# Kernel tuning notes

Measured on AMD Instinct MI355X. Metric: run time of the kernel, lower is better.

## Reference

```python
import jax, jax.numpy as jnp
import numpy as np

W_DIM = 512
IN_CH = 512
OUT_CH = 512
K = 3
PAD = K // 2
LR_MUL = 1.0
WEIGHT_GAIN = LR_MUL / np.sqrt(IN_CH * K * K)
MOD_WEIGHT_GAIN = 1.0 / np.sqrt(W_DIM)  # EqualizedLinear lr_mul=1.0
MOD_BIAS_GAIN = 1.0


def setup_inputs() -> dict:
    key = jax.random.key(0)
    k1, k2, k3, k4 = jax.random.split(key, 4)
    x = jax.random.normal(k1, (16, IN_CH, 64, 64), dtype=jnp.float32)
    w = jax.random.normal(k2, (16, W_DIM), dtype=jnp.float32)
    weight = jax.random.normal(k3, (OUT_CH, IN_CH, K, K), dtype=jnp.float32) / LR_MUL
    mod_weight = jax.random.normal(k4, (IN_CH, W_DIM), dtype=jnp.float32)
    mod_bias = jnp.ones((IN_CH,), dtype=jnp.float32)  # bias_init=1.0
    return {"x": x, "w": w, "weight": weight, "mod_weight": mod_weight, "mod_bias": mod_bias}


def _conv_one(xi, wi):
    # xi: [C_in, H, W], wi: [C_out, C_in, K, K]
    out = jax.lax.conv_general_dilated(
        xi[None], wi, window_strides=(1, 1),
        padding=[(PAD, PAD), (PAD, PAD)],
        dimension_numbers=("NCHW", "OIHW", "NCHW"))
    return out[0]


def reference(x, w, weight, mod_weight, mod_bias):
    # style = EqualizedLinear(w): [B, C_in]
    style = w @ (mod_weight * MOD_WEIGHT_GAIN).T + mod_bias * MOD_BIAS_GAIN
    # modulate weights per-sample: [B, C_out, C_in, K, K]
    wmod = (weight * WEIGHT_GAIN)[None] * style[:, None, :, None, None]
    # demodulate
    demod = jax.lax.rsqrt(jnp.sum(jnp.square(wmod), axis=(2, 3, 4), keepdims=True) + 1e-8)
    wmod = wmod * demod
    # per-sample conv (groups=batch in the original) via vmap
    out = jax.vmap(_conv_one)(x, wmod)  # [B, C_out, H, W]
    return out
```

## Files before the change

### kernel.cpp

```cpp
#include <hip/hip_runtime.h>
#include <hip/hip_bf16.h>

#define IN_CH 512
#define OUT_CH 512
#define HW 64
#define BATCH 16
#define WEIGHT_GAIN 0.014731391274719739f
#define MOD_WEIGHT_GAIN 0.04419417382415922f

#define PAD_W 66
#define XS_PIX_STRIDE 512

typedef __attribute__((ext_vector_type(8))) short frag8;
typedef __attribute__((ext_vector_type(4))) float f32x4;

__global__ void style_kernel(const float* __restrict__ w, const float* __restrict__ mw,
                             const float* __restrict__ mb, float* __restrict__ style) {
    const int gw = (blockIdx.x * 256 + threadIdx.x) >> 6;
    const int lane = threadIdx.x & 63;
    const int b = gw >> 9;
    const int i = gw & 511;
    const float4* mwp = (const float4*)(mw + (size_t)i * 512 + lane * 8);
    const float4* wp  = (const float4*)(w + (size_t)b * 512 + lane * 8);
    float4 m0 = mwp[0], m1 = mwp[1];
    float4 w0 = wp[0],  w1 = wp[1];
    float s = m0.x * w0.x + m0.y * w0.y + m0.z * w0.z + m0.w * w0.w
            + m1.x * w1.x + m1.y * w1.y + m1.z * w1.z + m1.w * w1.w;
#pragma unroll
    for (int off = 32; off > 0; off >>= 1) s += __shfl_down(s, off, 64);
    if (lane == 0) style[(size_t)b * 512 + i] = s * MOD_WEIGHT_GAIN + mb[i];
}

__global__ void wprep_kernel(const float* __restrict__ weight, float* __restrict__ wsq,
                             __hip_bfloat16* __restrict__ wbf) {
    const int idx = blockIdx.x * 256 + threadIdx.x;
    const float* wp = weight + idx * 9;
    float s = 0.f;
#pragma unroll
    for (int kk = 0; kk < 9; ++kk) {
        float v = wp[kk];
        s += v * v;
        wbf[kk * 262144 + idx] = __float2bfloat16(v);
    }
    wsq[idx] = s * (WEIGHT_GAIN * WEIGHT_GAIN);
}

__global__ void demod_kernel(const float* __restrict__ style, const float* __restrict__ wsq,
                             float* __restrict__ sc) {
    const int gw = (blockIdx.x * 256 + threadIdx.x) >> 6;
    const int lane = threadIdx.x & 63;
    const int b = gw >> 9;
    const int o = gw & 511;
    const float4* wq = (const float4*)(wsq + (size_t)o * 512 + lane * 8);
    const float4* st = (const float4*)(style + (size_t)b * 512 + lane * 8);
    float4 q0 = wq[0], q1 = wq[1];
    float4 s0 = st[0], s1 = st[1];
    float acc = q0.x * s0.x * s0.x + q0.y * s0.y * s0.y + q0.z * s0.z * s0.z + q0.w * s0.w * s0.w
              + q1.x * s1.x * s1.x + q1.y * s1.y * s1.y + q1.z * s1.z * s1.z + q1.w * s1.w * s1.w;
#pragma unroll
    for (int off = 32; off > 0; off >>= 1) acc += __shfl_down(acc, off, 64);
    if (lane == 0) sc[(size_t)b * 512 + o] = rsqrtf(acc + 1e-8f) * WEIGHT_GAIN;
}

__global__ void xs_kernel(const float* __restrict__ x, const float* __restrict__ style,
                          __hip_bfloat16* __restrict__ xsp) {
    const int y = blockIdx.x;
    const int b = blockIdx.z;
    const int t = threadIdx.x;
    const int lane = t & 63;
    const int j0 = (blockIdx.y * 4 + (t >> 6)) * 32;

    const float* xb = x + (((size_t)b * 512 + j0) * 64 + y) * 64 + lane;
    const float* stb = style + (size_t)b * 512 + j0;
    __hip_bfloat16* dst = xsp + (((size_t)b * PAD_W + (y + 1)) * PAD_W + (lane + 1)) * XS_PIX_STRIDE + j0;

    union { __hip_bfloat16 h[32]; uint4 u[4]; } pk;
#pragma unroll
    for (int k = 0; k < 32; ++k) {
        float v = xb[(size_t)k * 4096];
        pk.h[k] = __float2bfloat16(v * stb[k]);
    }
#pragma unroll
    for (int q = 0; q < 4; ++q) ((uint4*)dst)[q] = pk.u[q];
}

__global__ void border_kernel(__hip_bfloat16* __restrict__ xsp) {
    const int gw = (blockIdx.x * 256 + threadIdx.x) >> 6;
    const int lane = threadIdx.x & 63;
    const int b = gw / 260;
    const int p = gw % 260;
    int row, col;
    if (p < 66)       { row = 0;            col = p; }
    else if (p < 132) { row = 65;           col = p - 66; }
    else if (p < 196) { row = p - 132 + 1;  col = 0; }
    else              { row = p - 196 + 1;  col = 65; }
    uint4* dst = (uint4*)(xsp + (((size_t)b * PAD_W + row) * PAD_W + col) * XS_PIX_STRIDE);
    dst[lane] = uint4{0, 0, 0, 0};
}

__global__ void conv_kernel(const __hip_bfloat16* __restrict__ wbf,
                            const __hip_bfloat16* __restrict__ xsp,
                            const float* __restrict__ sc,
                            float* __restrict__ out) {
    __shared__ __hip_bfloat16 ash[128 * 64];
    __shared__ __hip_bfloat16 bsh[128 * 64];

    const int t = threadIdx.x;
    const int p0 = blockIdx.x * 128;
    const int m0 = blockIdx.y * 128;
    const int b  = blockIdx.z;
    const int y0 = p0 >> 6;

    const int r_base = t >> 3;
    const int s_slot = (t & 7) ^ (r_base & 7);
    const int aoff = (m0 + r_base) * 512 + s_slot * 8;
    int pixoff[4];
#pragma unroll
    for (int q = 0; q < 4; ++q) {
        const int rB = q * 32 + r_base;
        const int yy = y0 + (rB >> 6);
        const int xx = rB & 63;
        pixoff[q] = (((b * PAD_W) + yy) * PAD_W + xx) * XS_PIX_STRIDE + s_slot * 8;
    }

    const int wv = t >> 6;
    const int wm = (wv >> 1) * 64;
    const int wn = (wv & 1) * 64;
    const int lane = t & 63;
    const int ln15 = lane & 15;
    const int quad = lane >> 4;

    f32x4 acc[4][4] = {};

    const short* ashp = (const short*)ash;
    const short* bshp = (const short*)bsh;

    for (int kk = 0; kk < 9; ++kk) {
        const __hip_bfloat16* wsrc = wbf + kk * 262144 + aoff;
        const int shift = ((kk / 3) * PAD_W + (kk % 3)) * XS_PIX_STRIDE;
        const __hip_bfloat16* xbase = xsp + shift;

        for (int c0 = 0; c0 < 512; c0 += 64) {
#pragma unroll
            for (int q = 0; q < 4; ++q) {
                __builtin_amdgcn_global_load_lds(
                    (const __attribute__((address_space(1))) unsigned int*)(wsrc + q * 16384 + c0),
                    (__attribute__((address_space(3))) unsigned int*)((char*)ash + q * 4096 + t * 16),
                    16, 0, 0);
            }
#pragma unroll
            for (int q = 0; q < 4; ++q) {
                __builtin_amdgcn_global_load_lds(
                    (const __attribute__((address_space(1))) unsigned int*)(xbase + pixoff[q] + c0),
                    (__attribute__((address_space(3))) unsigned int*)((char*)bsh + q * 4096 + t * 16),
                    16, 0, 0);
            }
            __syncthreads();

#pragma unroll
            for (int ks = 0; ks < 2; ++ks) {
                const int gq = ks * 4 + quad;
                frag8 af[4], bfr[4];
#pragma unroll
                for (int mt = 0; mt < 4; ++mt) {
                    const int R = wm + mt * 16 + ln15;
                    af[mt] = *(const frag8*)(ashp + R * 64 + ((gq ^ (R & 7)) << 3));
                }
#pragma unroll
                for (int nt = 0; nt < 4; ++nt) {
                    const int R = wn + nt * 16 + ln15;
                    bfr[nt] = *(const frag8*)(bshp + R * 64 + ((gq ^ (R & 7)) << 3));
                }
#pragma unroll
                for (int mt = 0; mt < 4; ++mt)
#pragma unroll
                    for (int nt = 0; nt < 4; ++nt)
                        acc[mt][nt] = __builtin_amdgcn_mfma_f32_16x16x32_bf16(
                            af[mt], bfr[nt], acc[mt][nt], 0, 0, 0);
            }
            __syncthreads();
        }
    }

    const float* scb = sc + b * 512;
    float* outb = out + (size_t)b * 512 * 4096;
#pragma unroll
    for (int mt = 0; mt < 4; ++mt) {
        const int mrow = m0 + wm + mt * 16 + quad * 4;
#pragma unroll
        for (int v = 0; v < 4; ++v) {
            const float s = scb[mrow + v];
            float* orow = outb + (size_t)(mrow + v) * 4096 + p0 + wn + ln15;
#pragma unroll
            for (int nt = 0; nt < 4; ++nt)
                orow[nt * 16] = acc[mt][nt][v] * s;
        }
    }
}

extern "C" void kernel_launch(void* const* d_in, const int* in_sizes, int n_in,
                              void* d_out, int out_size, void* d_ws, size_t ws_size,
                              hipStream_t stream) {
    (void)in_sizes; (void)n_in; (void)out_size; (void)ws_size;
    const float* x      = (const float*)d_in[0];
    const float* w      = (const float*)d_in[1];
    const float* weight = (const float*)d_in[2];
    const float* mw     = (const float*)d_in[3];
    const float* mb     = (const float*)d_in[4];
    float* out = (float*)d_out;

    char* ws = (char*)d_ws;
    float* style         = (float*)(ws + 0);
    float* sc            = (float*)(ws + 32768);
    float* wsq           = (float*)(ws + 65536);
    __hip_bfloat16* wbf  = (__hip_bfloat16*)(ws + 1114112);
    __hip_bfloat16* xsp  = (__hip_bfloat16*)(ws + 5832704);

    wprep_kernel<<<dim3(1024), dim3(256), 0, stream>>>(weight, wsq, wbf);
    style_kernel<<<dim3(2048), dim3(256), 0, stream>>>(w, mw, mb, style);
    demod_kernel<<<dim3(2048), dim3(256), 0, stream>>>(style, wsq, sc);
    border_kernel<<<dim3(1040), dim3(256), 0, stream>>>(xsp);
    xs_kernel<<<dim3(64, 4, BATCH), dim3(256), 0, stream>>>(x, style, xsp);
    conv_kernel<<<dim3(32, 4, BATCH), dim3(256), 0, stream>>>(wbf, xsp, sc, out);
}
```

Baseline: 526.6 us.

## Fuse input modulation and padding into conv via shared halo slab

Removes the separate xs and border kernels. The conv kernel now loads fp32 x directly, multiplies by style, converts to bf16 and writes a 4-row by 66-column haloed slab per 64-channel chunk into LDS. All nine taps are then computed from that slab, so the input tile is reused across taps instead of reloaded per tap. Weight fragments are read straight from global memory into registers instead of being staged in LDS. This cuts the intermediate padded tensor round-trip but adds strided fp32 global reads of x (eight channel planes per thread) and uncached, uncoalesced A-fragment loads inside the MMA loop.

Measured after the change: 1.171 ms. 122% more time.

```diff
diff --git a/kernel.cpp b/kernel.cpp
--- a/kernel.cpp
+++ b/kernel.cpp
@@ -7,9 +7,6 @@
 #define BATCH 16
 #define WEIGHT_GAIN 0.014731391274719739f
 #define MOD_WEIGHT_GAIN 0.04419417382415922f
-
-#define PAD_W 66
-#define XS_PIX_STRIDE 512
 
 typedef __attribute__((ext_vector_type(8))) short frag8;
 typedef __attribute__((ext_vector_type(4))) float f32x4;
@@ -62,66 +59,22 @@
     if (lane == 0) sc[(size_t)b * 512 + o] = rsqrtf(acc + 1e-8f) * WEIGHT_GAIN;
 }
 
-__global__ void xs_kernel(const float* __restrict__ x, const float* __restrict__ style,
-                          __hip_bfloat16* __restrict__ xsp) {
-    const int y = blockIdx.x;
-    const int b = blockIdx.z;
-    const int t = threadIdx.x;
-    const int lane = t & 63;
-    const int j0 = (blockIdx.y * 4 + (t >> 6)) * 32;
-
-    const float* xb = x + (((size_t)b * 512 + j0) * 64 + y) * 64 + lane;
-    const float* stb = style + (size_t)b * 512 + j0;
-    __hip_bfloat16* dst = xsp + (((size_t)b * PAD_W + (y + 1)) * PAD_W + (lane + 1)) * XS_PIX_STRIDE + j0;
-
-    union { __hip_bfloat16 h[32]; uint4 u[4]; } pk;
-#pragma unroll
-    for (int k = 0; k < 32; ++k) {
-        float v = xb[(size_t)k * 4096];
-        pk.h[k] = __float2bfloat16(v * stb[k]);
-    }
-#pragma unroll
-    for (int q = 0; q < 4; ++q) ((uint4*)dst)[q] = pk.u[q];
-}
-
-__global__ void border_kernel(__hip_bfloat16* __restrict__ xsp) {
-    const int gw = (blockIdx.x * 256 + threadIdx.x) >> 6;
-    const int lane = threadIdx.x & 63;
-    const int b = gw / 260;
-    const int p = gw % 260;
-    int row, col;
-    if (p < 66)       { row = 0;            col = p; }
-    else if (p < 132) { row = 65;           col = p - 66; }
-    else if (p < 196) { row = p - 132 + 1;  col = 0; }
-    else              { row = p - 196 + 1;  col = 65; }
-    uint4* dst = (uint4*)(xsp + (((size_t)b * PAD_W + row) * PAD_W + col) * XS_PIX_STRIDE);
-    dst[lane] = uint4{0, 0, 0, 0};
-}
-
-__global__ void conv_kernel(const __hip_bfloat16* __restrict__ wbf,
-                            const __hip_bfloat16* __restrict__ xsp,
+__launch_bounds__(256, 3)
+__global__ void conv_kernel(const float* __restrict__ x,
+                            const __hip_bfloat16* __restrict__ wbf,
+                            const float* __restrict__ style,
                             const float* __restrict__ sc,
                             float* __restrict__ out) {
-    __shared__ __hip_bfloat16 ash[128 * 64];
-    __shared__ __hip_bfloat16 bsh[128 * 64];
+    __shared__ __hip_bfloat16 slab[264 * 64];
 
     const int t = threadIdx.x;
     const int p0 = blockIdx.x * 128;
     const int m0 = blockIdx.y * 128;
     const int b  = blockIdx.z;
-    const int y0 = p0 >> 6;
+    const int y0 = blockIdx.x * 2;
 
-    const int r_base = t >> 3;
-    const int s_slot = (t & 7) ^ (r_base & 7);
-    const int aoff = (m0 + r_base) * 512 + s_slot * 8;
-    int pixoff[4];
-#pragma unroll
-    for (int q = 0; q < 4; ++q) {
-        const int rB = q * 32 + r_base;
-        const int yy = y0 + (rB >> 6);
-        const int xx = rB & 63;
-        pixoff[q] = (((b * PAD_W) + yy) * PAD_W + xx) * XS_PIX_STRIDE + s_slot * 8;
-    }
+    const int sp = t & 31;
+    const int chunk = t >> 5;
 
     const int wv = t >> 6;
     const int wm = (wv >> 1) * 64;
@@ -129,56 +82,74 @@
     const int lane = t & 63;
     const int ln15 = lane & 15;
     const int quad = lane >> 4;
+    const int dy = wn >> 6;
+
+    const __hip_bfloat16* abase = wbf + (m0 + wm + ln15) * 512 + quad * 8;
+    const float* xb0 = x + (size_t)b * 512 * 4096;
+    const short* slabp = (const short*)slab;
 
     f32x4 acc[4][4] = {};
 
-    const short* ashp = (const short*)ash;
-    const short* bshp = (const short*)bsh;
+    for (int c0 = 0; c0 < 512; c0 += 64) {
+        const int ch0 = c0 + chunk * 8;
+        float st[8];
+#pragma unroll
+        for (int c = 0; c < 8; ++c) st[c] = style[b * 512 + ch0 + c];
 
-    for (int kk = 0; kk < 9; ++kk) {
-        const __hip_bfloat16* wsrc = wbf + kk * 262144 + aoff;
-        const int shift = ((kk / 3) * PAD_W + (kk % 3)) * XS_PIX_STRIDE;
-        const __hip_bfloat16* xbase = xsp + shift;
+        __syncthreads();
+#pragma unroll
+        for (int pass = 0; pass < 9; ++pass) {
+            const int p = pass * 32 + sp;
+            const bool pv = (p < 264);
+            const int r = p / 66;
+            const int cc = p - r * 66;
+            const int iy = y0 - 1 + r;
+            const int ix = cc - 1;
+            const bool valid = pv && (iy >= 0) && (iy < 64) && (ix >= 0) && (ix < 64);
+            const int cy = min(max(iy, 0), 63);
+            const int cx = min(max(ix, 0), 63);
+            const float* xb = xb0 + ((size_t)ch0 * 64 + cy) * 64 + cx;
+            union { __hip_bfloat16 h[8]; uint4 u[2]; } pk;
+#pragma unroll
+            for (int c = 0; c < 8; ++c) {
+                float v = xb[(size_t)c * 4096];
+                pk.h[c] = __float2bfloat16(valid ? v * st[c] : 0.f);
+            }
+            if (pv) {
+                uint4* dst = (uint4*)(slab + p * 64 + ((chunk ^ (p & 7)) << 3));
+                *dst = pk.u[0];
+            }
+            (void)pk.u[1];
+        }
+        __syncthreads();
 
-        for (int c0 = 0; c0 < 512; c0 += 64) {
 #pragma unroll
-            for (int q = 0; q < 4; ++q) {
-                __builtin_amdgcn_global_load_lds(
-                    (const __attribute__((address_space(1))) unsigned int*)(wsrc + q * 16384 + c0),
-                    (__attribute__((address_space(3))) unsigned int*)((char*)ash + q * 4096 + t * 16),
-                    16, 0, 0);
-            }
+        for (int kk = 0; kk < 9; ++kk) {
+            const int ky = kk / 3, kx = kk % 3;
+            const __hip_bfloat16* asrc = abase + kk * 262144 + c0;
+            frag8 af[2][4], bfr[2][4];
 #pragma unroll
-            for (int q = 0; q < 4; ++q) {
-                __builtin_amdgcn_global_load_lds(
-                    (const __attribute__((address_space(1))) unsigned int*)(xbase + pixoff[q] + c0),
-                    (__attribute__((address_space(3))) unsigned int*)((char*)bsh + q * 4096 + t * 16),
-                    16, 0, 0);
-            }
-            __syncthreads();
-
+            for (int ks = 0; ks < 2; ++ks)
+#pragma unroll
+                for (int mt = 0; mt < 4; ++mt)
+                    af[ks][mt] = *(const frag8*)(asrc + ks * 32 + mt * 8192);
 #pragma unroll
             for (int ks = 0; ks < 2; ++ks) {
                 const int gq = ks * 4 + quad;
-                frag8 af[4], bfr[4];
-#pragma unroll
-                for (int mt = 0; mt < 4; ++mt) {
-                    const int R = wm + mt * 16 + ln15;
-                    af[mt] = *(const frag8*)(ashp + R * 64 + ((gq ^ (R & 7)) << 3));
-                }
 #pragma unroll
                 for (int nt = 0; nt < 4; ++nt) {
-                    const int R = wn + nt * 16 + ln15;
-                    bfr[nt] = *(const frag8*)(bshp + R * 64 + ((gq ^ (R & 7)) << 3));
+                    const int p = (dy + ky) * 66 + nt * 16 + ln15 + kx;
+                    bfr[ks][nt] = *(const frag8*)(slabp + p * 64 + ((gq ^ (p & 7)) << 3));
                 }
+            }
 #pragma unroll
-                for (int mt = 0; mt < 4; ++mt)
+            for (int mt = 0; mt < 4; ++mt)
 #pragma unroll
-                    for (int nt = 0; nt < 4; ++nt)
+                for (int nt = 0; nt < 4; ++nt)
+#pragma unroll
+                    for (int ks = 0; ks < 2; ++ks)
                         acc[mt][nt] = __builtin_amdgcn_mfma_f32_16x16x32_bf16(
-                            af[mt], bfr[nt], acc[mt][nt], 0, 0, 0);
-            }
-            __syncthreads();
+                            af[ks][mt], bfr[ks][nt], acc[mt][nt], 0, 0, 0);
         }
     }
 
@@ -214,12 +185,9 @@
     float* sc            = (float*)(ws + 32768);
     float* wsq           = (float*)(ws + 65536);
     __hip_bfloat16* wbf  = (__hip_bfloat16*)(ws + 1114112);
-    __hip_bfloat16* xsp  = (__hip_bfloat16*)(ws + 5832704);
 
     wprep_kernel<<<dim3(1024), dim3(256), 0, stream>>>(weight, wsq, wbf);
     style_kernel<<<dim3(2048), dim3(256), 0, stream>>>(w, mw, mb, style);
     demod_kernel<<<dim3(2048), dim3(256), 0, stream>>>(style, wsq, sc);
-    border_kernel<<<dim3(1040), dim3(256), 0, stream>>>(xsp);
-    xs_kernel<<<dim3(64, 4, BATCH), dim3(256), 0, stream>>>(x, style, xsp);
-    conv_kernel<<<dim3(32, 4, BATCH), dim3(256), 0, stream>>>(wbf, xsp, sc, out);
+    conv_kernel<<<dim3(32, 4, BATCH), dim3(256), 0, stream>>>(x, wbf, style, sc, out);
 }
```
